# Optimization experiments

Measured on AMD Instinct MI355X. Metric: run time of the kernel, lower is better.

The kernel has to match this reference:

```python
import jax, jax.numpy as jnp
import numpy as np

B, S, T = 32, 128, 64
H = 512
VS = VT = 32000


def _lstm_cell(x, h, c, W, U, b):
    # Keras LSTM gate order: i, f, g(cell), o
    z = x @ W + h @ U + b
    i, f, g, o = jnp.split(z, 4, axis=-1)
    c = jax.nn.sigmoid(f) * c + jax.nn.sigmoid(i) * jnp.tanh(g)
    h = jax.nn.sigmoid(o) * jnp.tanh(c)
    return h, c


def _lstm_scan(xs, h0, c0, W, U, b):
    # xs: [S, B, D]
    def step(carry, x):
        h, c = _lstm_cell(x, carry[0], carry[1], W, U, b)
        return (h, c), h
    (hT, cT), hs = jax.lax.scan(step, (h0, c0), xs)
    return hs, hT, cT


def setup_inputs() -> dict:
    key = jax.random.key(0)
    ks = jax.random.split(key, 16)
    def n(k, shape, s=0.02):
        return (jax.random.normal(k, shape, jnp.float32) * s).astype(jnp.float32)
    return {
        "src": jax.random.randint(ks[0], (B, S), 0, VS, jnp.int32),
        "trg": jax.random.randint(ks[1], (B, T), 0, VT, jnp.int32),
        "E_src": n(ks[2], (VS, H)),
        "E_trg": n(ks[3], (VT, H)),
        "Wf": n(ks[4], (H, 4 * H)), "Uf": n(ks[5], (H, 4 * H)), "bf": jnp.zeros((4 * H,), jnp.float32),
        "Wb": n(ks[6], (H, 4 * H)), "Ub": n(ks[7], (H, 4 * H)), "bb": jnp.zeros((4 * H,), jnp.float32),
        "Wd": n(ks[8], (H, 4 * H)), "Ud": n(ks[9], (H, 4 * H)), "bd": jnp.zeros((4 * H,), jnp.float32),
        "fcW": n(ks[10], (2 * H, H)), "fcb": jnp.zeros((H,), jnp.float32),
        "clsW": n(ks[11], (2 * H, VT)), "clsb": jnp.zeros((VT,), jnp.float32),
    }


def reference(src, trg, E_src, E_trg, Wf, Uf, bf, Wb, Ub, bb, Wd, Ud, bd, fcW, fcb, clsW, clsb):
    Bn = src.shape[0]
    Hn = E_src.shape[1]
    # --- Encoder: bidirectional LSTM ---
    xs = E_src[src].transpose(1, 0, 2)          # [S, B, H]
    z0 = jnp.zeros((Bn, Hn), xs.dtype)
    hs_f, hf, cf = _lstm_scan(xs, z0, z0, Wf, Uf, bf)
    hs_b, hb, cb = _lstm_scan(xs[::-1], z0, z0, Wb, Ub, bb)
    src_hidden = jnp.concatenate([hs_f, hs_b[::-1]], axis=-1).transpose(1, 0, 2)  # [B, S, 2H]
    # --- shared fc projections (same Dense, 2H -> H) ---
    src_h = src_hidden @ fcW + fcb                                   # [B, S, H]
    prev_h = jnp.concatenate([hf, hb], axis=-1) @ fcW + fcb          # [B, H]
    prev_c = jnp.concatenate([cf, cb], axis=-1) @ fcW + fcb          # [B, H]
    neg = jnp.where(src == 0, jnp.float32(-1e9), jnp.float32(0.0))   # [B, S]
    # --- Decoder (teacher forcing): per-step LSTM cell + dot-product attention ---
    ys = E_trg[trg[:, :-1]].transpose(1, 0, 2)  # [T-1, B, H]

    def step(carry, x):
        h, c = _lstm_cell(x, carry[0], carry[1], Wd, Ud, bd)
        score = jnp.einsum('bh,bsh->bs', h, src_h) + neg
        attn = jax.nn.softmax(score, axis=-1)
        ws = jnp.einsum('bs,bsh->bh', attn, src_h)
        return (h, c), jnp.concatenate([ws, h], axis=-1)  # dec_state [B, 2H]

    _, dec = jax.lax.scan(step, (prev_h, prev_c), ys)     # [T-1, B, 2H]
    logits = dec.transpose(1, 0, 2) @ clsW + clsb          # [B, T-1, VT]
    return logits
```

## Files before the change

kernel.cpp:

```cpp
#include <hip/hip_runtime.h>
#include <hip/hip_bf16.h>
#include <stdint.h>
#include <string.h>

constexpr int cB = 32, cS = 128, cT = 64, cH = 512, cH4 = 2048, cVT = 32000, cTM1 = 63;

typedef __attribute__((ext_vector_type(8))) __bf16 bf16x8;
typedef __attribute__((ext_vector_type(4))) float f32x4;

__device__ __forceinline__ float sigm(float x) { return 1.0f / (1.0f + expf(-x)); }

__device__ __forceinline__ bf16x8 sc_load16(const __hip_bfloat16* p) {
  bf16x8 r;
  asm volatile("global_load_dwordx4 %0, %1, off sc0 sc1"
               : "=&v"(r) : "v"(p) : "memory");
  return r;
}
__device__ __forceinline__ void sc_store2(__hip_bfloat16* p, float hval) {
  __hip_bfloat16 hb = __float2bfloat16(hval);
  unsigned short us;
  memcpy(&us, &hb, 2);
  unsigned u = us;
  asm volatile("global_store_short %0, %1, off sc0 sc1"
               :: "v"(p), "v"(u) : "memory");
}

__device__ __forceinline__ void gridbar(unsigned* ctr, unsigned* flag,
                                        unsigned nblk, unsigned gen) {
  asm volatile("s_waitcnt vmcnt(0)" ::: "memory");
  __syncthreads();
  if (threadIdx.x == 0) {
    unsigned old = __hip_atomic_fetch_add(ctr, 1u, __ATOMIC_RELAXED,
                                          __HIP_MEMORY_SCOPE_AGENT);
    if (old == gen * nblk - 1u) {
      __hip_atomic_store(flag, gen, __ATOMIC_RELAXED, __HIP_MEMORY_SCOPE_AGENT);
    } else {
      while (__hip_atomic_load(flag, __ATOMIC_RELAXED, __HIP_MEMORY_SCOPE_AGENT) < gen)
        __builtin_amdgcn_s_sleep(2);
    }
  }
  __syncthreads();
}

__global__ __launch_bounds__(64) void k_init_bars(unsigned* p) {
  if (threadIdx.x < 16) p[threadIdx.x] = 0u;
}

__global__ __launch_bounds__(128) void k_embed_src(const int* __restrict__ src,
                                                   const float* __restrict__ E,
                                                   __hip_bfloat16* __restrict__ xs_bf,
                                                   float* __restrict__ neg) {
  int sb = blockIdx.x;
  int s = sb >> 5, b = sb & 31;
  int tok = src[b * cS + s];
  float4 e = ((const float4*)(E + (size_t)tok * cH))[threadIdx.x];
  __hip_bfloat16* drow = xs_bf + (size_t)sb * cH + threadIdx.x * 4;
  drow[0] = __float2bfloat16(e.x); drow[1] = __float2bfloat16(e.y);
  drow[2] = __float2bfloat16(e.z); drow[3] = __float2bfloat16(e.w);
  if (threadIdx.x == 0) neg[b * cS + s] = (tok == 0) ? -1e9f : 0.0f;
}

__global__ __launch_bounds__(128) void k_embed_trg(const int* __restrict__ trg,
                                                   const float* __restrict__ E,
                                                   __hip_bfloat16* __restrict__ ys_bf) {
  int tb = blockIdx.x;
  int t = tb >> 5, b = tb & 31;
  int tok = trg[b * cT + t];
  float4 e = ((const float4*)(E + (size_t)tok * cH))[threadIdx.x];
  __hip_bfloat16* drow = ys_bf + (size_t)tb * cH + threadIdx.x * 4;
  drow[0] = __float2bfloat16(e.x); drow[1] = __float2bfloat16(e.y);
  drow[2] = __float2bfloat16(e.z); drow[3] = __float2bfloat16(e.w);
}

__global__ __launch_bounds__(256) void k_f2b(const float* __restrict__ src,
                                             __hip_bfloat16* __restrict__ dst,
                                             int srcN, int dstN) {
  int i = blockIdx.x * 256 + threadIdx.x;
  if (i < dstN) {
    float v = (i < srcN) ? src[i] : 0.0f;
    dst[i] = __float2bfloat16(v);
  }
}

__global__ __launch_bounds__(256) void k_f2bT(const float* __restrict__ src,
                                              __hip_bfloat16* __restrict__ dst,
                                              int K, int N, int gi) {
  __shared__ float t[32][33];
  int nt = blockIdx.x * 32, kt = blockIdx.y * 32;
  int c = threadIdx.x & 31, r0 = threadIdx.x >> 5;
#pragma unroll
  for (int i = 0; i < 4; ++i) {
    int r = r0 + i * 8;
    t[r][c] = src[(size_t)(kt + r) * N + nt + c];
  }
  __syncthreads();
#pragma unroll
  for (int i = 0; i < 4; ++i) {
    int row = nt + r0 + i * 8;
    int pr = gi ? (((row & 511) << 2) | (row >> 9)) : row;
    dst[(size_t)pr * K + kt + c] = __float2bfloat16(t[c][r0 + i * 8]);
  }
}

__global__ __launch_bounds__(256) void k_permb(const float* __restrict__ in,
                                               float* __restrict__ out) {
  int i = blockIdx.x * 256 + threadIdx.x;
  out[i] = in[(i & 3) * 512 + (i >> 2)];
}

__global__ __launch_bounds__(256) void k_bgemm(const __hip_bfloat16* __restrict__ A,
                                               const __hip_bfloat16* __restrict__ Bt,
                                               const float* __restrict__ bias,
                                               float* __restrict__ C,
                                               int M, int K, int N) {
  __shared__ __hip_bfloat16 As[128 * 64];
  __shared__ __hip_bfloat16 Bs[128 * 64];
  const int tid = threadIdx.x;
  const int lane = tid & 63;
  const int wave = tid >> 6;
  const int wr = wave >> 1, wc = wave & 1;
  const int bm = blockIdx.x * 128, bn = blockIdx.y * 128;

  f32x4 acc[4][4] = {};

  const int srow = lane >> 3;
  const int scol = (lane & 7) * 8;

  for (int kt = 0; kt < K; kt += 64) {
#pragma unroll
    for (int i = 0; i < 4; ++i) {
      int c = wave * 4 + i;
      const __hip_bfloat16* ga = A + (size_t)(bm + c * 8 + srow) * K + kt + scol;
      __builtin_amdgcn_global_load_lds(
          (const __attribute__((address_space(1))) uint32_t*)ga,
          (__attribute__((address_space(3))) uint32_t*)(As + c * 512), 16, 0, 0);
      const __hip_bfloat16* gb = Bt + (size_t)(bn + c * 8 + srow) * K + kt + scol;
      __builtin_amdgcn_global_load_lds(
          (const __attribute__((address_space(1))) uint32_t*)gb,
          (__attribute__((address_space(3))) uint32_t*)(Bs + c * 512), 16, 0, 0);
    }
    __syncthreads();

#pragma unroll
    for (int kk = 0; kk < 64; kk += 32) {
      const int ko = kk + (lane >> 4) * 8;
      bf16x8 a[4], b[4];
      const int ar = wr * 64 + (lane & 15);
#pragma unroll
      for (int m = 0; m < 4; ++m)
        a[m] = *(const bf16x8*)(As + (size_t)(ar + m * 16) * 64 + ko);
      const int br = wc * 64 + (lane & 15);
#pragma unroll
      for (int n = 0; n < 4; ++n)
        b[n] = *(const bf16x8*)(Bs + (size_t)(br + n * 16) * 64 + ko);
#pragma unroll
      for (int m = 0; m < 4; ++m)
#pragma unroll
        for (int n = 0; n < 4; ++n)
          acc[m][n] = __builtin_amdgcn_mfma_f32_16x16x32_bf16(a[m], b[n], acc[m][n], 0, 0, 0);
    }
    __syncthreads();
  }

#pragma unroll
  for (int m = 0; m < 4; ++m) {
    const int row0 = bm + wr * 64 + m * 16 + (lane >> 4) * 4;
#pragma unroll
    for (int n = 0; n < 4; ++n) {
      const int col = bn + wc * 64 + n * 16 + (lane & 15);
      const float bv = bias[col];
#pragma unroll
      for (int r = 0; r < 4; ++r) {
        const int row = row0 + r;
        if (row < M) C[(size_t)row * N + col] = acc[m][n][r] + bv;
      }
    }
  }
}

__global__ __launch_bounds__(256, 1) void k_enc_mfma(
    const float* __restrict__ xWf, const float* __restrict__ xWb,
    const __hip_bfloat16* __restrict__ Utf, const __hip_bfloat16* __restrict__ Utb,
    __hip_bfloat16* __restrict__ hs_f, __hip_bfloat16* __restrict__ hs_b,
    __hip_bfloat16* __restrict__ henc,
    float* __restrict__ cf, float* __restrict__ cb,
    unsigned* bars) {
  const int bid = blockIdx.x;
  const int dir = bid >> 5, nb = bid & 31;
  const int c0 = nb * 64;
  const float* xW = dir ? xWb : xWf;
  const __hip_bfloat16* Ut = dir ? Utb : Utf;
  __hip_bfloat16* hs = dir ? hs_b : hs_f;
  __hip_bfloat16* hcur = henc + (size_t)dir * 32768;
  float* cOut = dir ? cb : cf;
  unsigned* ctr = bars + dir * 2;
  unsigned* flag = bars + dir * 2 + 1;

  __shared__ __hip_bfloat16 Hs[32][520];
  __shared__ float Zs[32][68];

  const int tid = threadIdx.x;
  const int lane = tid & 63;
  const int wv = tid >> 6;
  const int wm = wv >> 1, wn = wv & 1;
  const int fr = lane & 15;
  const int fq = lane >> 4;

  bf16x8 bfrag[2][16];
#pragma unroll
  for (int n = 0; n < 2; ++n)
#pragma unroll
    for (int kk = 0; kk < 16; ++kk)
      bfrag[n][kk] = *(const bf16x8*)(Ut + (size_t)(c0 + (wn * 2 + n) * 16 + fr) * 512 + kk * 32 + fq * 8);

  const int b0 = tid >> 4;
  const int jj = tid & 15;
  const int jglob = nb * 16 + jj;
  float cs0 = 0.f, cs1 = 0.f;

  const int trow0 = dir ? 127 : 0;
  float4 z0 = *(const float4*)(xW + ((size_t)(trow0 * 32 + b0)) * 2048 + c0 + 4 * jj);
  float4 z1 = *(const float4*)(xW + ((size_t)(trow0 * 32 + b0 + 16)) * 2048 + c0 + 4 * jj);

  for (int t = 0; t < 128; ++t) {
    const int trow = dir ? (127 - t) : t;
    if (t > 0) {
      const __hip_bfloat16* hsrc = hcur + (size_t)((t + 1) & 1) * 16384;
      bf16x8 hr[8];
#pragma unroll
      for (int i = 0; i < 8; ++i) {
        int c = tid + i * 256;
        hr[i] = sc_load16(hsrc + (size_t)c * 8);
      }
      asm volatile("s_waitcnt vmcnt(0)" ::: "memory");
      __builtin_amdgcn_sched_barrier(0);
#pragma unroll
      for (int i = 0; i < 8; ++i) {
        int c = tid + i * 256;
        int r = c >> 6, cc = (c & 63) * 8;
        *(bf16x8*)&Hs[r][cc] = hr[i];
      }
    }
    const int tn = (t < 127) ? t + 1 : 127;
    const int ntrow = dir ? (127 - tn) : tn;
    float4 zn0 = *(const float4*)(xW + ((size_t)(ntrow * 32 + b0)) * 2048 + c0 + 4 * jj);
    float4 zn1 = *(const float4*)(xW + ((size_t)(ntrow * 32 + b0 + 16)) * 2048 + c0 + 4 * jj);

    asm volatile("s_waitcnt lgkmcnt(0)" ::: "memory");
    __builtin_amdgcn_s_barrier();
    __builtin_amdgcn_sched_barrier(0);

    if (t > 0) {
      f32x4 acc0 = {}, acc1 = {};
#pragma unroll
      for (int kk = 0; kk < 16; ++kk) {
        bf16x8 a = *(const bf16x8*)&Hs[wm * 16 + fr][kk * 32 + fq * 8];
        acc0 = __builtin_amdgcn_mfma_f32_16x16x32_bf16(a, bfrag[0][kk], acc0, 0, 0, 0);
        acc1 = __builtin_amdgcn_mfma_f32_16x16x32_bf16(a, bfrag[1][kk], acc1, 0, 0, 0);
      }
#pragma unroll
      for (int r = 0; r < 4; ++r) {
        Zs[wm * 16 + fq * 4 + r][(wn * 2 + 0) * 16 + fr] = acc0[r];
        Zs[wm * 16 + fq * 4 + r][(wn * 2 + 1) * 16 + fr] = acc1[r];
      }
    }
    asm volatile("s_waitcnt lgkmcnt(0)" ::: "memory");
    __builtin_amdgcn_s_barrier();
    __builtin_amdgcn_sched_barrier(0);

    {
      float4 z = z0;
      if (t > 0) { float4 q = *(const float4*)&Zs[b0][4 * jj]; z.x += q.x; z.y += q.y; z.z += q.z; z.w += q.w; }
      cs0 = sigm(z.y) * cs0 + sigm(z.x) * tanhf(z.z);
      float h = sigm(z.w) * tanhf(cs0);
      sc_store2(hcur + (size_t)(t & 1) * 16384 + (size_t)b0 * 512 + jglob, h);
      hs[((size_t)trow * 32 + b0) * 512 + jglob] = __float2bfloat16(h);
    }
    {
      int b1 = b0 + 16;
      float4 z = z1;
      if (t > 0) { float4 q = *(const float4*)&Zs[b1][4 * jj]; z.x += q.x; z.y += q.y; z.z += q.z; z.w += q.w; }
      cs1 = sigm(z.y) * cs1 + sigm(z.x) * tanhf(z.z);
      float h = sigm(z.w) * tanhf(cs1);
      sc_store2(hcur + (size_t)(t & 1) * 16384 + (size_t)b1 * 512 + jglob, h);
      hs[((size_t)trow * 32 + b1) * 512 + jglob] = __float2bfloat16(h);
    }
    z0 = zn0; z1 = zn1;
    if (t < 127) gridbar(ctr, flag, 32u, (unsigned)(t + 1));
  }
  cOut[(size_t)b0 * 512 + jglob] = cs0;
  cOut[(size_t)(b0 + 16) * 512 + jglob] = cs1;
}

__global__ __launch_bounds__(256, 1) void k_dec_mfma(
    const float* __restrict__ yW, const __hip_bfloat16* __restrict__ Utd,
    const float* __restrict__ prev_c,
    __hip_bfloat16* __restrict__ hdec, __hip_bfloat16* __restrict__ decb,
    unsigned* ctr, unsigned* flag) {
  const int nb = blockIdx.x;
  const int c0 = nb * 64;

  __shared__ __hip_bfloat16 Hs[32][520];
  __shared__ float Zs[32][68];

  const int tid = threadIdx.x;
  const int lane = tid & 63;
  const int wv = tid >> 6;
  const int wm = wv >> 1, wn = wv & 1;
  const int fr = lane & 15;
  const int fq = lane >> 4;

  bf16x8 bfrag[2][16];
#pragma unroll
  for (int n = 0; n < 2; ++n)
#pragma unroll
    for (int kk = 0; kk < 16; ++kk)
      bfrag[n][kk] = *(const bf16x8*)(Utd + (size_t)(c0 + (wn * 2 + n) * 16 + fr) * 512 + kk * 32 + fq * 8);

  const int b0 = tid >> 4;
  const int jj = tid & 15;
  const int jglob = nb * 16 + jj;
  float cs0 = prev_c[(size_t)b0 * 512 + jglob];
  float cs1 = prev_c[(size_t)(b0 + 16) * 512 + jglob];

  float4 z0 = *(const float4*)(yW + ((size_t)b0) * 2048 + c0 + 4 * jj);
  float4 z1 = *(const float4*)(yW + ((size_t)(b0 + 16)) * 2048 + c0 + 4 * jj);

  for (int t = 0; t < cTM1; ++t) {
    const __hip_bfloat16* hsrc = hdec + (size_t)((t + 1) & 1) * 16384;
    {
      bf16x8 hr[8];
#pragma unroll
      for (int i = 0; i < 8; ++i) {
        int c = tid + i * 256;
        hr[i] = sc_load16(hsrc + (size_t)c * 8);
      }
      asm volatile("s_waitcnt vmcnt(0)" ::: "memory");
      __builtin_amdgcn_sched_barrier(0);
#pragma unroll
      for (int i = 0; i < 8; ++i) {
        int c = tid + i * 256;
        int r = c >> 6, cc = (c & 63) * 8;
        *(bf16x8*)&Hs[r][cc] = hr[i];
      }
    }
    const int tn = (t < cTM1 - 1) ? t + 1 : cTM1 - 1;
    float4 zn0 = *(const float4*)(yW + ((size_t)(tn * 32 + b0)) * 2048 + c0 + 4 * jj);
    float4 zn1 = *(const float4*)(yW + ((size_t)(tn * 32 + b0 + 16)) * 2048 + c0 + 4 * jj);

    asm volatile("s_waitcnt lgkmcnt(0)" ::: "memory");
    __builtin_amdgcn_s_barrier();
    __builtin_amdgcn_sched_barrier(0);

    {
      f32x4 acc0 = {}, acc1 = {};
#pragma unroll
      for (int kk = 0; kk < 16; ++kk) {
        bf16x8 a = *(const bf16x8*)&Hs[wm * 16 + fr][kk * 32 + fq * 8];
        acc0 = __builtin_amdgcn_mfma_f32_16x16x32_bf16(a, bfrag[0][kk], acc0, 0, 0, 0);
        acc1 = __builtin_amdgcn_mfma_f32_16x16x32_bf16(a, bfrag[1][kk], acc1, 0, 0, 0);
      }
#pragma unroll
      for (int r = 0; r < 4; ++r) {
        Zs[wm * 16 + fq * 4 + r][(wn * 2 + 0) * 16 + fr] = acc0[r];
        Zs[wm * 16 + fq * 4 + r][(wn * 2 + 1) * 16 + fr] = acc1[r];
      }
    }
    asm volatile("s_waitcnt lgkmcnt(0)" ::: "memory");
    __builtin_amdgcn_s_barrier();
    __builtin_amdgcn_sched_barrier(0);

    {
      float4 z = z0;
      float4 q = *(const float4*)&Zs[b0][4 * jj];
      z.x += q.x; z.y += q.y; z.z += q.z; z.w += q.w;
      cs0 = sigm(z.y) * cs0 + sigm(z.x) * tanhf(z.z);
      float h = sigm(z.w) * tanhf(cs0);
      sc_store2(hdec + (size_t)(t & 1) * 16384 + (size_t)b0 * 512 + jglob, h);
      decb[((size_t)b0 * cTM1 + t) * 1024 + 512 + jglob] = __float2bfloat16(h);
    }
    {
      int b1 = b0 + 16;
      float4 z = z1;
      float4 q = *(const float4*)&Zs[b1][4 * jj];
      z.x += q.x; z.y += q.y; z.z += q.z; z.w += q.w;
      cs1 = sigm(z.y) * cs1 + sigm(z.x) * tanhf(z.z);
      float h = sigm(z.w) * tanhf(cs1);
      sc_store2(hdec + (size_t)(t & 1) * 16384 + (size_t)b1 * 512 + jglob, h);
      decb[((size_t)b1 * cTM1 + t) * 1024 + 512 + jglob] = __float2bfloat16(h);
    }
    z0 = zn0; z1 = zn1;
    if (t < cTM1 - 1) gridbar(ctr, flag, 32u, (unsigned)(t + 1));
  }
}

__global__ __launch_bounds__(128) void k_cat_bf(const __hip_bfloat16* __restrict__ hs_f,
                                                const __hip_bfloat16* __restrict__ hs_b,
                                                const float* __restrict__ cf,
                                                const float* __restrict__ cb,
                                                __hip_bfloat16* __restrict__ cat) {
  int r = blockIdx.x;
  int tid = threadIdx.x;
  __hip_bfloat16* drow = cat + (size_t)r * 1024 + tid * 8;
  if (r >= 4160) {
    bf16x8 zv = {};
    *(bf16x8*)drow = zv;
    return;
  }
  if (r < 4128) {
    const __hip_bfloat16 *pf, *pb;
    if (r < 4096) {
      int b = r >> 7, s = r & 127;
      pf = hs_f + ((size_t)s * 32 + b) * 512;
      pb = hs_b + ((size_t)s * 32 + b) * 512;
    } else {
      int b = r - 4096;
      pf = hs_f + ((size_t)127 * 32 + b) * 512;
      pb = hs_b + ((size_t)b) * 512;
    }
    const __hip_bfloat16* s8 = (tid < 64) ? (pf + tid * 8) : (pb + (tid - 64) * 8);
    *(bf16x8*)drow = *(const bf16x8*)s8;
  } else {
    int b = r - 4128;
    const float* s8 = (tid < 64) ? (cf + (size_t)b * 512 + tid * 8)
                                 : (cb + (size_t)b * 512 + (tid - 64) * 8);
    bf16x8 v;
#pragma unroll
    for (int i = 0; i < 8; ++i) v[i] = (__bf16)s8[i];
    *(bf16x8*)drow = v;
  }
}

__global__ __launch_bounds__(256) void k_attn_all(const float* __restrict__ src_h,
                                                  const float* __restrict__ neg,
                                                  __hip_bfloat16* __restrict__ decb) {
  int bid = blockIdx.x;
  int xcd = bid & 7, idx = bid >> 3;
  int b = xcd + 8 * (idx / 63);
  int t = idx % 63;
  int tx = threadIdx.x;
  __shared__ float hv[cH];
  __shared__ float part[256];
  __shared__ float sc[cS];
  __shared__ float red[cS];
  __hip_bfloat16* drow = decb + ((size_t)b * cTM1 + t) * (2 * cH);
  hv[tx] = __bfloat162float(drow[cH + tx]);
  hv[tx + 256] = __bfloat162float(drow[cH + tx + 256]);
  __syncthreads();
  {
    int s = tx >> 1, half = tx & 1;
    const float4* sr = (const float4*)(src_h + ((size_t)b * cS + s) * cH + half * 256);
    const float4* hh = (const float4*)(hv + half * 256);
    float acc = 0.f;
#pragma unroll 8
    for (int k = 0; k < 64; ++k) {
      float4 v = sr[k], h4 = hh[k];
      acc += v.x * h4.x + v.y * h4.y + v.z * h4.z + v.w * h4.w;
    }
    part[tx] = acc;
  }
  __syncthreads();
  if (tx < cS) {
    float s0 = part[2 * tx] + part[2 * tx + 1] + neg[b * cS + tx];
    sc[tx] = s0;
    red[tx] = s0;
  }
  __syncthreads();
  for (int off = 64; off >= 1; off >>= 1) {
    if (tx < off) red[tx] = fmaxf(red[tx], red[tx + off]);
    __syncthreads();
  }
  float mx = red[0];
  __syncthreads();
  float e = 0.f;
  if (tx < cS) { e = expf(sc[tx] - mx); red[tx] = e; }
  __syncthreads();
  for (int off = 64; off >= 1; off >>= 1) {
    if (tx < off) red[tx] += red[tx + off];
    __syncthreads();
  }
  float inv = 1.0f / red[0];
  __syncthreads();
  if (tx < cS) sc[tx] = e * inv;
  __syncthreads();
  float a0 = 0.f, a1 = 0.f;
  for (int s = 0; s < cS; ++s) {
    float w = sc[s];
    const float* sr = src_h + ((size_t)b * cS + s) * cH;
    a0 += w * sr[tx];
    a1 += w * sr[tx + 256];
  }
  drow[tx] = __float2bfloat16(a0);
  drow[tx + 256] = __float2bfloat16(a1);
}

extern "C" void kernel_launch(void* const* d_in, const int* in_sizes, int n_in,
                              void* d_out, int out_size, void* d_ws, size_t ws_size,
                              hipStream_t stream) {
  const int* src = (const int*)d_in[0];
  const int* trg = (const int*)d_in[1];
  const float* E_src = (const float*)d_in[2];
  const float* E_trg = (const float*)d_in[3];
  const float* Wf = (const float*)d_in[4];
  const float* Uf = (const float*)d_in[5];
  const float* bf = (const float*)d_in[6];
  const float* Wb = (const float*)d_in[7];
  const float* Ub = (const float*)d_in[8];
  const float* bb = (const float*)d_in[9];
  const float* Wd = (const float*)d_in[10];
  const float* Ud = (const float*)d_in[11];
  const float* bd = (const float*)d_in[12];
  const float* fcW = (const float*)d_in[13];
  const float* fcb = (const float*)d_in[14];
  const float* clsW = (const float*)d_in[15];
  const float* clsb = (const float*)d_in[16];
  float* out = (float*)d_out;
  float* ws = (float*)d_ws;

  float* xWf = ws;
  float* xWb = ws + 8388608;
  float* yW = ws + 16777216;
  __hip_bfloat16* hs_f = (__hip_bfloat16*)(ws + 20905984);
  __hip_bfloat16* hs_b = (__hip_bfloat16*)(ws + 21954560);
  float* cf = ws + 23003136;
  float* cb = ws + 23019520;
  float* neg = ws + 23035904;
  float* fco = ws + 23040000;
  __hip_bfloat16* decb = (__hip_bfloat16*)(ws + 25169920);
  __hip_bfloat16* Utd = (__hip_bfloat16*)(ws + 26218496);
  __hip_bfloat16* henc = (__hip_bfloat16*)(ws + 26742784);
  __hip_bfloat16* hdec = (__hip_bfloat16*)(ws + 26808320);
  unsigned* bars = (unsigned*)(ws + 26841088);
  float* pool = ws + 26841152;

  __hip_bfloat16* xs_bf = (__hip_bfloat16*)pool;
  __hip_bfloat16* ys_bf = (__hip_bfloat16*)(pool + 1048576);
  __hip_bfloat16* Utf = (__hip_bfloat16*)(pool + 1572864);
  __hip_bfloat16* Utb = (__hip_bfloat16*)(pool + 2097152);
  __hip_bfloat16* Wtfx = (__hip_bfloat16*)(pool + 2621440);
  __hip_bfloat16* Wtbx = (__hip_bfloat16*)(pool + 3145728);
  __hip_bfloat16* Wtdx = (__hip_bfloat16*)(pool + 3670016);
  float* bfx = pool + 4194304;
  float* bbx = pool + 4196352;
  float* bdx = pool + 4198400;
  __hip_bfloat16* cat_bf = (__hip_bfloat16*)pool;
  __hip_bfloat16* fcWt = (__hip_bfloat16*)(pool + 2162688);
  __hip_bfloat16* clsWt = (__hip_bfloat16*)xWf;

  k_embed_src<<<4096, 128, 0, stream>>>(src, E_src, xs_bf, neg);
  k_embed_trg<<<2016, 128, 0, stream>>>(trg, E_trg, ys_bf);
  k_f2b<<<64, 256, 0, stream>>>(nullptr, ys_bf + (size_t)2016 * 512, 0, 16384);
  k_f2bT<<<dim3(64, 16), 256, 0, stream>>>(Wf, Wtfx, 512, 2048, 1);
  k_f2bT<<<dim3(64, 16), 256, 0, stream>>>(Wb, Wtbx, 512, 2048, 1);
  k_f2bT<<<dim3(64, 16), 256, 0, stream>>>(Wd, Wtdx, 512, 2048, 1);
  k_f2bT<<<dim3(64, 16), 256, 0, stream>>>(Uf, Utf, 512, 2048, 1);
  k_f2bT<<<dim3(64, 16), 256, 0, stream>>>(Ub, Utb, 512, 2048, 1);
  k_f2bT<<<dim3(64, 16), 256, 0, stream>>>(Ud, Utd, 512, 2048, 1);
  k_permb<<<8, 256, 0, stream>>>(bf, bfx);
  k_permb<<<8, 256, 0, stream>>>(bb, bbx);
  k_permb<<<8, 256, 0, stream>>>(bd, bdx);

  k_bgemm<<<dim3(32, 16), 256, 0, stream>>>(xs_bf, Wtfx, bfx, xWf, 4096, 512, 2048);
  k_bgemm<<<dim3(32, 16), 256, 0, stream>>>(xs_bf, Wtbx, bbx, xWb, 4096, 512, 2048);
  k_bgemm<<<dim3(16, 16), 256, 0, stream>>>(ys_bf, Wtdx, bdx, yW, 2016, 512, 2048);

  k_init_bars<<<1, 64, 0, stream>>>(bars);
  k_enc_mfma<<<64, 256, 0, stream>>>(xWf, xWb, Utf, Utb, hs_f, hs_b, henc, cf, cb, bars);

  k_cat_bf<<<4224, 128, 0, stream>>>(hs_f, hs_b, cf, cb, cat_bf);
  k_f2bT<<<dim3(16, 32), 256, 0, stream>>>(fcW, fcWt, 1024, 512, 0);
  k_bgemm<<<dim3(33, 4), 256, 0, stream>>>(cat_bf, fcWt, fcb, fco, 4160, 1024, 512);

  k_f2bT<<<dim3(1000, 32), 256, 0, stream>>>(clsW, clsWt, 1024, 32000, 0);

  const float* prev_h = fco + (size_t)4096 * 512;
  const float* prev_c = fco + (size_t)4128 * 512;
  k_f2b<<<64, 256, 0, stream>>>(prev_h, hdec + 16384, 16384, 16384);
  k_dec_mfma<<<32, 256, 0, stream>>>(yW, Utd, prev_c, hdec, decb, bars + 4, bars + 5);
  k_attn_all<<<2016, 256, 0, stream>>>(fco, neg, decb);

  k_bgemm<<<dim3(16, 250), 256, 0, stream>>>(decb, clsWt, clsb, out, 2016, 1024, 32000);
}
```

Measured before the change: 1.358 ms.

## Fuse prep kernels, drop LDS gate staging in LSTM loops, overlap clsW transpose

Merges the many weight-transpose, bias-permute and zero-pad launches into one k_prep kernel. In both recurrent kernels the MFMA operands are swapped so each lane directly holds the four gate values it needs, removing the Zs shared-memory round trip and one barrier per step. The decoder seeds its first hidden state from prev_h itself instead of using a separate conversion launch. Extra blocks in the decoder launch perform the large clsW transpose alongside the serial recurrence, and the grid-barrier spin sleep is shortened. The risks are extra blocks competing with the latency-bound recurrence for memory bandwidth, and a co-residency requirement for the spin-barrier blocks.

Measured after the change: 1.392 ms. 1.02x slower.

```diff
diff --git a/kernel.cpp b/kernel.cpp
--- a/kernel.cpp
+++ b/kernel.cpp
@@ -36,7 +36,7 @@
       __hip_atomic_store(flag, gen, __ATOMIC_RELAXED, __HIP_MEMORY_SCOPE_AGENT);
     } else {
       while (__hip_atomic_load(flag, __ATOMIC_RELAXED, __HIP_MEMORY_SCOPE_AGENT) < gen)
-        __builtin_amdgcn_s_sleep(2);
+        __builtin_amdgcn_s_sleep(1);
     }
   }
   __syncthreads();
@@ -72,21 +72,11 @@
   drow[2] = __float2bfloat16(e.z); drow[3] = __float2bfloat16(e.w);
 }
 
-__global__ __launch_bounds__(256) void k_f2b(const float* __restrict__ src,
-                                             __hip_bfloat16* __restrict__ dst,
-                                             int srcN, int dstN) {
-  int i = blockIdx.x * 256 + threadIdx.x;
-  if (i < dstN) {
-    float v = (i < srcN) ? src[i] : 0.0f;
-    dst[i] = __float2bfloat16(v);
-  }
-}
-
-__global__ __launch_bounds__(256) void k_f2bT(const float* __restrict__ src,
-                                              __hip_bfloat16* __restrict__ dst,
-                                              int K, int N, int gi) {
-  __shared__ float t[32][33];
-  int nt = blockIdx.x * 32, kt = blockIdx.y * 32;
+__device__ __forceinline__ void f2bT_tile(const float* __restrict__ src,
+                                          __hip_bfloat16* __restrict__ dst,
+                                          int K, int N, int gi, int bx, int by,
+                                          float (*t)[33]) {
+  int nt = bx * 32, kt = by * 32;
   int c = threadIdx.x & 31, r0 = threadIdx.x >> 5;
 #pragma unroll
   for (int i = 0; i < 4; ++i) {
@@ -100,12 +90,48 @@
     int pr = gi ? (((row & 511) << 2) | (row >> 9)) : row;
     dst[(size_t)pr * K + kt + c] = __float2bfloat16(t[c][r0 + i * 8]);
   }
-}
-
-__global__ __launch_bounds__(256) void k_permb(const float* __restrict__ in,
-                                               float* __restrict__ out) {
-  int i = blockIdx.x * 256 + threadIdx.x;
-  out[i] = in[(i & 3) * 512 + (i >> 2)];
+  __syncthreads();
+}
+
+__global__ __launch_bounds__(256) void k_prep(
+    const float* __restrict__ Wf, const float* __restrict__ Wb, const float* __restrict__ Wd,
+    const float* __restrict__ Uf, const float* __restrict__ Ub, const float* __restrict__ Ud,
+    const float* __restrict__ fcW,
+    const float* __restrict__ bf, const float* __restrict__ bb, const float* __restrict__ bd,
+    __hip_bfloat16* __restrict__ Wtfx, __hip_bfloat16* __restrict__ Wtbx,
+    __hip_bfloat16* __restrict__ Wtdx,
+    __hip_bfloat16* __restrict__ Utf, __hip_bfloat16* __restrict__ Utb,
+    __hip_bfloat16* __restrict__ Utd,
+    __hip_bfloat16* __restrict__ fcWt,
+    float* __restrict__ bfx, float* __restrict__ bbx, float* __restrict__ bdx,
+    __hip_bfloat16* __restrict__ ys_pad) {
+  __shared__ float t[32][33];
+  int id = blockIdx.x;
+  if (id < 6144) {
+    int grp = id >> 10, r = id & 1023;
+    const float* s; __hip_bfloat16* d;
+    switch (grp) {
+      case 0: s = Wf; d = Wtfx; break;
+      case 1: s = Wb; d = Wtbx; break;
+      case 2: s = Wd; d = Wtdx; break;
+      case 3: s = Uf; d = Utf; break;
+      case 4: s = Ub; d = Utb; break;
+      default: s = Ud; d = Utd; break;
+    }
+    f2bT_tile(s, d, 512, 2048, 1, r & 63, r >> 6, t);
+  } else if (id < 6656) {
+    int r = id - 6144;
+    f2bT_tile(fcW, fcWt, 1024, 512, 0, r & 15, r >> 4, t);
+  } else if (id < 6680) {
+    int r = id - 6656;
+    const float* s = (r < 8) ? bf : ((r < 16) ? bb : bd);
+    float* d = (r < 8) ? bfx : ((r < 16) ? bbx : bdx);
+    int i = (r & 7) * 256 + threadIdx.x;
+    d[i] = s[(i & 3) * 512 + (i >> 2)];
+  } else {
+    int r = id - 6680;
+    ys_pad[r * 256 + threadIdx.x] = __float2bfloat16(0.0f);
+  }
 }
 
 __global__ __launch_bounds__(256) void k_bgemm(const __hip_bfloat16* __restrict__ A,
@@ -197,30 +223,26 @@
   unsigned* flag = bars + dir * 2 + 1;
 
   __shared__ __hip_bfloat16 Hs[32][520];
-  __shared__ float Zs[32][68];
 
   const int tid = threadIdx.x;
   const int lane = tid & 63;
   const int wv = tid >> 6;
-  const int wm = wv >> 1, wn = wv & 1;
   const int fr = lane & 15;
   const int fq = lane >> 4;
 
-  bf16x8 bfrag[2][16];
-#pragma unroll
-  for (int n = 0; n < 2; ++n)
-#pragma unroll
-    for (int kk = 0; kk < 16; ++kk)
-      bfrag[n][kk] = *(const bf16x8*)(Ut + (size_t)(c0 + (wn * 2 + n) * 16 + fr) * 512 + kk * 32 + fq * 8);
-
-  const int b0 = tid >> 4;
-  const int jj = tid & 15;
-  const int jglob = nb * 16 + jj;
+  bf16x8 afrag[16];
+#pragma unroll
+  for (int kk = 0; kk < 16; ++kk)
+    afrag[kk] = *(const bf16x8*)(Ut + (size_t)(c0 + wv * 16 + fr) * 512 + kk * 32 + fq * 8);
+
+  const int jglob = nb * 16 + wv * 4 + fq;
+  const int b0 = fr, b1 = fr + 16;
+  const int zc = c0 + wv * 16 + fq * 4;
   float cs0 = 0.f, cs1 = 0.f;
 
   const int trow0 = dir ? 127 : 0;
-  float4 z0 = *(const float4*)(xW + ((size_t)(trow0 * 32 + b0)) * 2048 + c0 + 4 * jj);
-  float4 z1 = *(const float4*)(xW + ((size_t)(trow0 * 32 + b0 + 16)) * 2048 + c0 + 4 * jj);
+  float4 z0 = *(const float4*)(xW + ((size_t)(trow0 * 32 + b0)) * 2048 + zc);
+  float4 z1 = *(const float4*)(xW + ((size_t)(trow0 * 32 + b1)) * 2048 + zc);
 
   for (int t = 0; t < 128; ++t) {
     const int trow = dir ? (127 - t) : t;
@@ -243,45 +265,33 @@
     }
     const int tn = (t < 127) ? t + 1 : 127;
     const int ntrow = dir ? (127 - tn) : tn;
-    float4 zn0 = *(const float4*)(xW + ((size_t)(ntrow * 32 + b0)) * 2048 + c0 + 4 * jj);
-    float4 zn1 = *(const float4*)(xW + ((size_t)(ntrow * 32 + b0 + 16)) * 2048 + c0 + 4 * jj);
-
-    asm volatile("s_waitcnt lgkmcnt(0)" ::: "memory");
-    __builtin_amdgcn_s_barrier();
-    __builtin_amdgcn_sched_barrier(0);
-
+    float4 zn0 = *(const float4*)(xW + ((size_t)(ntrow * 32 + b0)) * 2048 + zc);
+    float4 zn1 = *(const float4*)(xW + ((size_t)(ntrow * 32 + b1)) * 2048 + zc);
+
+    f32x4 acc0 = {}, acc1 = {};
     if (t > 0) {
-      f32x4 acc0 = {}, acc1 = {};
+      asm volatile("s_waitcnt lgkmcnt(0)" ::: "memory");
+      __builtin_amdgcn_s_barrier();
+      __builtin_amdgcn_sched_barrier(0);
 #pragma unroll
       for (int kk = 0; kk < 16; ++kk) {
-        bf16x8 a = *(const bf16x8*)&Hs[wm * 16 + fr][kk * 32 + fq * 8];
-        acc0 = __builtin_amdgcn_mfma_f32_16x16x32_bf16(a, bfrag[0][kk], acc0, 0, 0, 0);
-        acc1 = __builtin_amdgcn_mfma_f32_16x16x32_bf16(a, bfrag[1][kk], acc1, 0, 0, 0);
-      }
-#pragma unroll
-      for (int r = 0; r < 4; ++r) {
-        Zs[wm * 16 + fq * 4 + r][(wn * 2 + 0) * 16 + fr] = acc0[r];
-        Zs[wm * 16 + fq * 4 + r][(wn * 2 + 1) * 16 + fr] = acc1[r];
-      }
-    }
-    asm volatile("s_waitcnt lgkmcnt(0)" ::: "memory");
-    __builtin_amdgcn_s_barrier();
-    __builtin_amdgcn_sched_barrier(0);
-
+        bf16x8 h0v = *(const bf16x8*)&Hs[b0][kk * 32 + fq * 8];
+        bf16x8 h1v = *(const bf16x8*)&Hs[b1][kk * 32 + fq * 8];
+        acc0 = __builtin_amdgcn_mfma_f32_16x16x32_bf16(afrag[kk], h0v, acc0, 0, 0, 0);
+        acc1 = __builtin_amdgcn_mfma_f32_16x16x32_bf16(afrag[kk], h1v, acc1, 0, 0, 0);
+      }
+    }
     {
-      float4 z = z0;
-      if (t > 0) { float4 q = *(const float4*)&Zs[b0][4 * jj]; z.x += q.x; z.y += q.y; z.z += q.z; z.w += q.w; }
-      cs0 = sigm(z.y) * cs0 + sigm(z.x) * tanhf(z.z);
-      float h = sigm(z.w) * tanhf(cs0);
+      float zi = z0.x + acc0[0], zf = z0.y + acc0[1], zg = z0.z + acc0[2], zo = z0.w + acc0[3];
+      cs0 = sigm(zf) * cs0 + sigm(zi) * tanhf(zg);
+      float h = sigm(zo) * tanhf(cs0);
       sc_store2(hcur + (size_t)(t & 1) * 16384 + (size_t)b0 * 512 + jglob, h);
       hs[((size_t)trow * 32 + b0) * 512 + jglob] = __float2bfloat16(h);
     }
     {
-      int b1 = b0 + 16;
-      float4 z = z1;
-      if (t > 0) { float4 q = *(const float4*)&Zs[b1][4 * jj]; z.x += q.x; z.y += q.y; z.z += q.z; z.w += q.w; }
-      cs1 = sigm(z.y) * cs1 + sigm(z.x) * tanhf(z.z);
-      float h = sigm(z.w) * tanhf(cs1);
+      float zi = z1.x + acc1[0], zf = z1.y + acc1[1], zg = z1.z + acc1[2], zo = z1.w + acc1[3];
+      cs1 = sigm(zf) * cs1 + sigm(zi) * tanhf(zg);
+      float h = sigm(zo) * tanhf(cs1);
       sc_store2(hcur + (size_t)(t & 1) * 16384 + (size_t)b1 * 512 + jglob, h);
       hs[((size_t)trow * 32 + b1) * 512 + jglob] = __float2bfloat16(h);
     }
@@ -289,46 +299,63 @@
     if (t < 127) gridbar(ctr, flag, 32u, (unsigned)(t + 1));
   }
   cOut[(size_t)b0 * 512 + jglob] = cs0;
-  cOut[(size_t)(b0 + 16) * 512 + jglob] = cs1;
+  cOut[(size_t)b1 * 512 + jglob] = cs1;
 }
 
 __global__ __launch_bounds__(256, 1) void k_dec_mfma(
     const float* __restrict__ yW, const __hip_bfloat16* __restrict__ Utd,
-    const float* __restrict__ prev_c,
+    const float* __restrict__ prev_h, const float* __restrict__ prev_c,
     __hip_bfloat16* __restrict__ hdec, __hip_bfloat16* __restrict__ decb,
+    const float* __restrict__ clsW, __hip_bfloat16* __restrict__ clsWt,
     unsigned* ctr, unsigned* flag) {
+  __shared__ __hip_bfloat16 Hs[32][520];
+  __shared__ float tt[32][33];
+
+  if (blockIdx.x >= 32) {
+    for (int tile = blockIdx.x - 32; tile < 32000; tile += (int)gridDim.x - 32) {
+      int bx = tile % 1000, by = tile / 1000;
+      f2bT_tile(clsW, clsWt, 1024, 32000, 0, bx, by, tt);
+    }
+    return;
+  }
+
   const int nb = blockIdx.x;
   const int c0 = nb * 64;
-
-  __shared__ __hip_bfloat16 Hs[32][520];
-  __shared__ float Zs[32][68];
-
   const int tid = threadIdx.x;
   const int lane = tid & 63;
   const int wv = tid >> 6;
-  const int wm = wv >> 1, wn = wv & 1;
   const int fr = lane & 15;
   const int fq = lane >> 4;
 
-  bf16x8 bfrag[2][16];
-#pragma unroll
-  for (int n = 0; n < 2; ++n)
-#pragma unroll
-    for (int kk = 0; kk < 16; ++kk)
-      bfrag[n][kk] = *(const bf16x8*)(Utd + (size_t)(c0 + (wn * 2 + n) * 16 + fr) * 512 + kk * 32 + fq * 8);
-
-  const int b0 = tid >> 4;
-  const int jj = tid & 15;
-  const int jglob = nb * 16 + jj;
+  bf16x8 afrag[16];
+#pragma unroll
+  for (int kk = 0; kk < 16; ++kk)
+    afrag[kk] = *(const bf16x8*)(Utd + (size_t)(c0 + wv * 16 + fr) * 512 + kk * 32 + fq * 8);
+
+  const int jglob = nb * 16 + wv * 4 + fq;
+  const int b0 = fr, b1 = fr + 16;
+  const int zc = c0 + wv * 16 + fq * 4;
   float cs0 = prev_c[(size_t)b0 * 512 + jglob];
-  float cs1 = prev_c[(size_t)(b0 + 16) * 512 + jglob];
-
-  float4 z0 = *(const float4*)(yW + ((size_t)b0) * 2048 + c0 + 4 * jj);
-  float4 z1 = *(const float4*)(yW + ((size_t)(b0 + 16)) * 2048 + c0 + 4 * jj);
+  float cs1 = prev_c[(size_t)b1 * 512 + jglob];
+
+  float4 z0 = *(const float4*)(yW + ((size_t)b0) * 2048 + zc);
+  float4 z1 = *(const float4*)(yW + ((size_t)b1) * 2048 + zc);
 
   for (int t = 0; t < cTM1; ++t) {
-    const __hip_bfloat16* hsrc = hdec + (size_t)((t + 1) & 1) * 16384;
-    {
+    if (t == 0) {
+      const float4* ph4 = (const float4*)prev_h;
+#pragma unroll
+      for (int i = 0; i < 16; ++i) {
+        int c = tid + i * 256;
+        float4 v = ph4[c];
+        int r = c >> 7, c4 = (c & 127) * 4;
+        Hs[r][c4 + 0] = __float2bfloat16(v.x);
+        Hs[r][c4 + 1] = __float2bfloat16(v.y);
+        Hs[r][c4 + 2] = __float2bfloat16(v.z);
+        Hs[r][c4 + 3] = __float2bfloat16(v.w);
+      }
+    } else {
+      const __hip_bfloat16* hsrc = hdec + (size_t)((t + 1) & 1) * 16384;
       bf16x8 hr[8];
 #pragma unroll
       for (int i = 0; i < 8; ++i) {
@@ -345,47 +372,32 @@
       }
     }
     const int tn = (t < cTM1 - 1) ? t + 1 : cTM1 - 1;
-    float4 zn0 = *(const float4*)(yW + ((size_t)(tn * 32 + b0)) * 2048 + c0 + 4 * jj);
-    float4 zn1 = *(const float4*)(yW + ((size_t)(tn * 32 + b0 + 16)) * 2048 + c0 + 4 * jj);
+    float4 zn0 = *(const float4*)(yW + ((size_t)(tn * 32 + b0)) * 2048 + zc);
+    float4 zn1 = *(const float4*)(yW + ((size_t)(tn * 32 + b1)) * 2048 + zc);
 
     asm volatile("s_waitcnt lgkmcnt(0)" ::: "memory");
     __builtin_amdgcn_s_barrier();
     __builtin_amdgcn_sched_barrier(0);
 
+    f32x4 acc0 = {}, acc1 = {};
+#pragma unroll
+    for (int kk = 0; kk < 16; ++kk) {
+      bf16x8 h0v = *(const bf16x8*)&Hs[b0][kk * 32 + fq * 8];
+      bf16x8 h1v = *(const bf16x8*)&Hs[b1][kk * 32 + fq * 8];
+      acc0 = __builtin_amdgcn_mfma_f32_16x16x32_bf16(afrag[kk], h0v, acc0, 0, 0, 0);
+      acc1 = __builtin_amdgcn_mfma_f32_16x16x32_bf16(afrag[kk], h1v, acc1, 0, 0, 0);
+    }
     {
-      f32x4 acc0 = {}, acc1 = {};
-#pragma unroll
-      for (int kk = 0; kk < 16; ++kk) {
-        bf16x8 a = *(const bf16x8*)&Hs[wm * 16 + fr][kk * 32 + fq * 8];
-        acc0 = __builtin_amdgcn_mfma_f32_16x16x32_bf16(a, bfrag[0][kk], acc0, 0, 0, 0);
-        acc1 = __builtin_amdgcn_mfma_f32_16x16x32_bf16(a, bfrag[1][kk], acc1, 0, 0, 0);
-      }
-#pragma unroll
-      for (int r = 0; r < 4; ++r) {
-        Zs[wm * 16 + fq * 4 + r][(wn * 2 + 0) * 16 + fr] = acc0[r];
-        Zs[wm * 16 + fq * 4 + r][(wn * 2 + 1) * 16 + fr] = acc1[r];
-      }
-    }
-    asm volatile("s_waitcnt lgkmcnt(0)" ::: "memory");
-    __builtin_amdgcn_s_barrier();
-    __builtin_amdgcn_sched_barrier(0);
-
-    {
-      float4 z = z0;
-      float4 q = *(const float4*)&Zs[b0][4 * jj];
-      z.x += q.x; z.y += q.y; z.z += q.z; z.w += q.w;
-      cs0 = sigm(z.y) * cs0 + sigm(z.x) * tanhf(z.z);
-      float h = sigm(z.w) * tanhf(cs0);
+      float zi = z0.x + acc0[0], zf = z0.y + acc0[1], zg = z0.z + acc0[2], zo = z0.w + acc0[3];
+      cs0 = sigm(zf) * cs0 + sigm(zi) * tanhf(zg);
+      float h = sigm(zo) * tanhf(cs0);
       sc_store2(hdec + (size_t)(t & 1) * 16384 + (size_t)b0 * 512 + jglob, h);
       decb[((size_t)b0 * cTM1 + t) * 1024 + 512 + jglob] = __float2bfloat16(h);
     }
     {
-      int b1 = b0 + 16;
-      float4 z = z1;
-      float4 q = *(const float4*)&Zs[b1][4 * jj];
-      z.x += q.x; z.y += q.y; z.z += q.z; z.w += q.w;
-      cs1 = sigm(z.y) * cs1 + sigm(z.x) * tanhf(z.z);
-      float h = sigm(z.w) * tanhf(cs1);
+      float zi = z1.x + acc1[0], zf = z1.y + acc1[1], zg = z1.z + acc1[2], zo = z1.w + acc1[3];
+      cs1 = sigm(zf) * cs1 + sigm(zi) * tanhf(zg);
+      float h = sigm(zo) * tanhf(cs1);
       sc_store2(hdec + (size_t)(t & 1) * 16384 + (size_t)b1 * 512 + jglob, h);
       decb[((size_t)b1 * cTM1 + t) * 1024 + 512 + jglob] = __float2bfloat16(h);
     }
@@ -543,22 +555,15 @@
   float* bfx = pool + 4194304;
   float* bbx = pool + 4196352;
   float* bdx = pool + 4198400;
+  __hip_bfloat16* fcWt = (__hip_bfloat16*)(pool + 4200448);
   __hip_bfloat16* cat_bf = (__hip_bfloat16*)pool;
-  __hip_bfloat16* fcWt = (__hip_bfloat16*)(pool + 2162688);
   __hip_bfloat16* clsWt = (__hip_bfloat16*)xWf;
 
   k_embed_src<<<4096, 128, 0, stream>>>(src, E_src, xs_bf, neg);
   k_embed_trg<<<2016, 128, 0, stream>>>(trg, E_trg, ys_bf);
-  k_f2b<<<64, 256, 0, stream>>>(nullptr, ys_bf + (size_t)2016 * 512, 0, 16384);
-  k_f2bT<<<dim3(64, 16), 256, 0, stream>>>(Wf, Wtfx, 512, 2048, 1);
-  k_f2bT<<<dim3(64, 16), 256, 0, stream>>>(Wb, Wtbx, 512, 2048, 1);
-  k_f2bT<<<dim3(64, 16), 256, 0, stream>>>(Wd, Wtdx, 512, 2048, 1);
-  k_f2bT<<<dim3(64, 16), 256, 0, stream>>>(Uf, Utf, 512, 2048, 1);
-  k_f2bT<<<dim3(64, 16), 256, 0, stream>>>(Ub, Utb, 512, 2048, 1);
-  k_f2bT<<<dim3(64, 16), 256, 0, stream>>>(Ud, Utd, 512, 2048, 1);
-  k_permb<<<8, 256, 0, stream>>>(bf, bfx);
-  k_permb<<<8, 256, 0, stream>>>(bb, bbx);
-  k_permb<<<8, 256, 0, stream>>>(bd, bdx);
+  k_prep<<<6744, 256, 0, stream>>>(Wf, Wb, Wd, Uf, Ub, Ud, fcW, bf, bb, bd,
+                                   Wtfx, Wtbx, Wtdx, Utf, Utb, Utd, fcWt,
+                                   bfx, bbx, bdx, ys_bf + (size_t)2016 * 512);
 
   k_bgemm<<<dim3(32, 16), 256, 0, stream>>>(xs_bf, Wtfx, bfx, xWf, 4096, 512, 2048);
   k_bgemm<<<dim3(32, 16), 256, 0, stream>>>(xs_bf, Wtbx, bbx, xWb, 4096, 512, 2048);
@@ -568,15 +573,12 @@
   k_enc_mfma<<<64, 256, 0, stream>>>(xWf, xWb, Utf, Utb, hs_f, hs_b, henc, cf, cb, bars);
 
   k_cat_bf<<<4224, 128, 0, stream>>>(hs_f, hs_b, cf, cb, cat_bf);
-  k_f2bT<<<dim3(16, 32), 256, 0, stream>>>(fcW, fcWt, 1024, 512, 0);
   k_bgemm<<<dim3(33, 4), 256, 0, stream>>>(cat_bf, fcWt, fcb, fco, 4160, 1024, 512);
-
-  k_f2bT<<<dim3(1000, 32), 256, 0, stream>>>(clsW, clsWt, 1024, 32000, 0);
 
   const float* prev_h = fco + (size_t)4096 * 512;
   const float* prev_c = fco + (size_t)4128 * 512;
-  k_f2b<<<64, 256, 0, stream>>>(prev_h, hdec + 16384, 16384, 16384);
-  k_dec_mfma<<<32, 256, 0, stream>>>(yW, Utd, prev_c, hdec, decb, bars + 4, bars + 5);
+  k_dec_mfma<<<256, 256, 0, stream>>>(yW, Utd, prev_h, prev_c, hdec, decb,
+                                      clsW, clsWt, bars + 4, bars + 5);
   k_attn_all<<<2016, 256, 0, stream>>>(fco, neg, decb);
 
   k_bgemm<<<dim3(16, 250), 256, 0, stream>>>(decb, clsWt, clsb, out, 2016, 1024, 32000);
```
